# Performance work log

Measured on AMD Instinct MI355X. Metric: run time of the kernel, lower is better.

## Reference

```python
import jax, jax.numpy as jnp
import numpy as np

MIN_SPARSITY = 0.05
MAX_SPARSITY = 0.3


def setup_inputs() -> dict:
    key = jax.random.key(0)
    k1, k2, k3 = jax.random.split(key, 3)
    B, D = 4096, 4096
    H = D // 4
    x = jax.random.normal(k1, (B, D), dtype=jnp.float32)
    W1 = jax.random.normal(k2, (D, H), dtype=jnp.float32) * (1.0 / np.sqrt(D))
    b1 = jnp.zeros((H,), dtype=jnp.float32)
    W2 = jax.random.normal(k3, (H, 1), dtype=jnp.float32) * (1.0 / np.sqrt(H))
    b2 = jnp.zeros((1,), dtype=jnp.float32)
    return {"x": x, "W1": W1, "b1": b1, "W2": W2, "b2": b2}


def reference(x, W1, b1, W2, b2):
    B, D = x.shape
    # learned per-row sparsity in [min, max]
    h = jax.nn.relu(x @ W1 + b1)                      # [B, D//4]
    s = jax.nn.sigmoid(h @ W2 + b2)                   # [B, 1]
    sparsity = MIN_SPARSITY + (MAX_SPARSITY - MIN_SPARSITY) * s  # [B, 1]

    # per-row kth smallest |x| as threshold; k = max(1, round(D*(1-sparsity)))
    abs_x = jnp.abs(x)
    sorted_abs = jnp.sort(abs_x, axis=1)              # [B, D] ascending
    k = jnp.round(D * (1.0 - sparsity[:, 0])).astype(jnp.int32)
    k = jnp.clip(k, 1, D)
    threshold = jnp.take_along_axis(sorted_abs, (k - 1)[:, None], axis=1)  # [B, 1]

    mask = (abs_x > threshold).astype(x.dtype)        # [B, D]
    sparse_x = x * mask
    actual_sparsity = mask.sum(axis=1) / D            # [B]
    l1_reg = jnp.abs(sparse_x).sum(axis=1).mean()     # scalar
    return sparse_x, mask, sparsity, actual_sparsity, l1_reg
```

## Files before the change

### kernel.cpp

```cpp
#include <hip/hip_runtime.h>
#include <hip/hip_fp8.h>

typedef __attribute__((ext_vector_type(4))) float f32x4;


__device__ __forceinline__ unsigned char f2fp8(float f) {
    return (unsigned char)__hip_cvt_float_to_fp8(f, __HIP_SATFINITE, __HIP_E4M3);
}

__device__ __forceinline__ void gl16(const void* g, void* l) {
    __builtin_amdgcn_global_load_lds(
        (const __attribute__((address_space(1))) void*)g,
        (__attribute__((address_space(3))) void*)l, 16, 0, 0);
}

__global__ __launch_bounds__(256) void k0a_cvtx(const float* __restrict__ x,
                                                unsigned char* __restrict__ xa_t)
{
    const int bm = blockIdx.x;
    const int ktbase = blockIdx.y * 16;
    const int t = threadIdx.x;
    const int rr = t >> 2, q = t & 3;
    const int kgp = q ^ ((rr >> 1) & 3);
    const size_t rowoff = (size_t)(bm * 64 + rr) * 4096;

    #pragma unroll
    for (int i = 0; i < 16; i++) {
        const int kt = ktbase + i;
        const float* src = x + rowoff + kt * 32 + q * 8;
        float4 v0 = *(const float4*)src;
        float4 v1 = *(const float4*)(src + 4);
        union { unsigned char c[8]; uint2 u; } o;
        o.c[0] = f2fp8(v0.x); o.c[1] = f2fp8(v0.y);
        o.c[2] = f2fp8(v0.z); o.c[3] = f2fp8(v0.w);
        o.c[4] = f2fp8(v1.x); o.c[5] = f2fp8(v1.y);
        o.c[6] = f2fp8(v1.z); o.c[7] = f2fp8(v1.w);
        *(uint2*)(xa_t + ((size_t)(bm * 128 + kt) * 64 + rr) * 32 + kgp * 8) = o.u;
    }
}

__global__ __launch_bounds__(256) void k0b_cvtw(const float* __restrict__ W1,
                                                unsigned char* __restrict__ wb_t)
{
    __shared__ float ls[32][128];
    const int bx = blockIdx.x;
    const int bn = bx >> 7, kt = bx & 127;
    const int t = threadIdx.x;

    #pragma unroll
    for (int i = 0; i < 4; i++) {
        int s = t + i * 256;
        int r = s >> 5, c4 = s & 31;
        *(float4*)&ls[r][c4 * 4] =
            *(const float4*)(W1 + (size_t)(kt * 32 + r) * 1024 + bn * 128 + c4 * 4);
    }
    __syncthreads();

    const int n = t >> 1, half = t & 1;
    #pragma unroll
    for (int kg2 = 0; kg2 < 2; kg2++) {
        const int kg = half * 2 + kg2;
        const int kgp = kg ^ ((n >> 1) & 3);
        union { unsigned char c[8]; uint2 u; } o;
        #pragma unroll
        for (int j = 0; j < 8; j++) o.c[j] = f2fp8(ls[kg * 8 + j][n] * 64.0f);
        *(uint2*)(wb_t + (size_t)(bn * 128 + kt) * 4096 + n * 32 + kgp * 8) = o.u;
    }
}

__global__ __launch_bounds__(256, 2) void k1est(const unsigned char* __restrict__ xa_t,
                                                const unsigned char* __restrict__ wb_t,
                                                const float* __restrict__ b1,
                                                const float* __restrict__ W2,
                                                float* __restrict__ plogit)
{
    __shared__ alignas(16) unsigned char Ab[4][4096];
    __shared__ alignas(16) unsigned char Bb[4][8192];

    const int bid = blockIdx.x;
    const int wgid = (bid & 7) * 64 + (bid >> 3);
    const int bn = wgid >> 6, bm = wgid & 63;
    const int tid = threadIdx.x;
    const int l = tid & 63, w = tid >> 6;
    const int arow = l & 15, kg = l >> 4;
    const int kgs = kg ^ ((arow >> 1) & 3);

    const unsigned char* abase = xa_t + (size_t)bm * 128 * 2048;
    const unsigned char* bbase = wb_t + (size_t)bn * 128 * 4096;

    f32x4 acc[8];
    #pragma unroll
    for (int j = 0; j < 8; j++) acc[j] = (f32x4)0.0f;

#define ISSUE(step, buf)                                                          \
    do {                                                                          \
        gl16(abase + (size_t)(step) * 4096 + tid * 16, &Ab[buf][tid * 16]);       \
        gl16(bbase + (size_t)(step) * 8192 + tid * 16, &Bb[buf][tid * 16]);       \
        gl16(bbase + (size_t)(step) * 8192 + (256 + tid) * 16,                    \
             &Bb[buf][(256 + tid) * 16]);                                         \
    } while (0)

    ISSUE(0, 0);
    ISSUE(1, 1);

    for (int t = 0; t < 64; t++) {
        const int buf = t & 3;
        if (t <= 61) {
            ISSUE(t + 2, (t + 2) & 3);
            asm volatile("s_waitcnt vmcnt(6)" ::: "memory");
        } else if (t == 62) {
            asm volatile("s_waitcnt vmcnt(3)" ::: "memory");
        } else {
            asm volatile("s_waitcnt vmcnt(0)" ::: "memory");
        }
        __builtin_amdgcn_s_barrier();
        __builtin_amdgcn_sched_barrier(0);

        #pragma unroll
        for (int j = 0; j < 2; j++) {
            long af = *(const long*)&Ab[buf][j * 2048 + (w * 16 + arow) * 32 + kgs * 8];
            #pragma unroll
            for (int nf = 0; nf < 8; nf++) {
                long bf = *(const long*)&Bb[buf][j * 4096 + (nf * 16 + arow) * 32 + kgs * 8];
                acc[nf] = __builtin_amdgcn_mfma_f32_16x16x32_fp8_fp8(af, bf, acc[nf], 0, 0, 0);
            }
        }
    }
#undef ISSUE

    float p[4] = {0.0f, 0.0f, 0.0f, 0.0f};
    #pragma unroll
    for (int nf = 0; nf < 8; nf++) {
        const int n = bn * 128 + nf * 16 + arow;
        const float bb = b1[n], ww = W2[n];
        #pragma unroll
        for (int i = 0; i < 4; i++) {
            float h = acc[nf][i] * 0.015625f + bb;
            if (h > 0.0f) p[i] += h * ww;
        }
    }
    #pragma unroll
    for (int i = 0; i < 4; i++) {
        #pragma unroll
        for (int o = 1; o < 16; o <<= 1) p[i] += __shfl_xor(p[i], o, 64);
        if (arow == 0) {
            const int row = bm * 64 + w * 16 + kg * 4 + i;
            plogit[(size_t)row * 8 + bn] = p[i];
        }
    }
}

__global__ __launch_bounds__(256) void k1b_k(const float* __restrict__ plogit,
                                             const float* __restrict__ b2,
                                             int* __restrict__ k_arr,
                                             float* __restrict__ sp_arr)
{
    int row = blockIdx.x * 256 + threadIdx.x;
    float lg = 0.0f;
    #pragma unroll
    for (int t = 0; t < 8; t++) lg += plogit[(size_t)row * 8 + t];
    double s  = 1.0 / (1.0 + exp(-(double)(lg + b2[0])));
    double sp = 0.05 + 0.25 * s;
    int k = (int)rint(4096.0 * (1.0 - sp));
    if (k < 1) k = 1;
    if (k > 4096) k = 4096;
    k_arr[row] = k;
    sp_arr[row] = (float)sp;
}

__global__ __launch_bounds__(256) void k2_row(const float* __restrict__ x,
                                              const int* __restrict__ k_arr,
                                              const float* __restrict__ sp_arr,
                                              float* __restrict__ out_sparse,
                                              float* __restrict__ out_mask,
                                              float* __restrict__ out_spars,
                                              float* __restrict__ out_actual,
                                              double* __restrict__ l1rows)
{
    __shared__ unsigned bits[4096];
    __shared__ unsigned hist[2048];
    __shared__ unsigned wsum[4];
    __shared__ int cnt_w[4];
    __shared__ double l1_w[4];
    __shared__ unsigned sel_s, selexc_s;

    const int row = blockIdx.x;
    const int tid = threadIdx.x;
    const int lane = tid & 63, wid = tid >> 6;
    const float* xr = x + (size_t)row * 4096;

    for (int i = tid; i < 1024; i += 256) {
        uint4 v = ((const uint4*)xr)[i];
        bits[i * 4 + 0] = v.x;
        bits[i * 4 + 1] = v.y;
        bits[i * 4 + 2] = v.z;
        bits[i * 4 + 3] = v.w;
    }
    if (tid == 0) out_spars[row] = sp_arr[row];

    int krem = k_arr[row];
    unsigned prefix = 0;

    for (int i = tid; i < 2048; i += 256) hist[i] = 0;
    __syncthreads();
    for (int i = tid; i < 4096; i += 256)
        atomicAdd(&hist[(bits[i] & 0x7fffffffu) >> 20], 1u);
    __syncthreads();
    {
        const unsigned base = tid * 8;
        unsigned bl[8];
        unsigned v = 0;
        #pragma unroll
        for (int j = 0; j < 8; j++) { bl[j] = hist[base + j]; v += bl[j]; }
        unsigned sc = v;
        #pragma unroll
        for (int o = 1; o < 64; o <<= 1) {
            unsigned n = __shfl_up(sc, o, 64);
            if (lane >= o) sc += n;
        }
        if (lane == 63) wsum[wid] = sc;
        __syncthreads();
        unsigned off = 0;
        for (int ww = 0; ww < wid; ww++) off += wsum[ww];
        sc += off;
        unsigned exc = sc - v;
        if ((int)sc >= krem && (int)exc < krem) {
            unsigned run = exc;
            #pragma unroll
            for (int j = 0; j < 8; j++) {
                if ((int)run < krem && (int)(run + bl[j]) >= krem) {
                    sel_s = base + j; selexc_s = run;
                }
                run += bl[j];
            }
        }
        __syncthreads();
        prefix = sel_s;
        krem -= (int)selexc_s;
        __syncthreads();
    }

    #pragma unroll
    for (int p = 0; p < 3; p++) {
        const int shift = (p == 0) ? 12 : (p == 1) ? 4 : 0;
        const int width = (p == 2) ? 4 : 8;
        const int nb = 1 << width;
        const int topshift = shift + width;
        if (tid < nb) hist[tid] = 0;
        __syncthreads();
        for (int i = tid; i < 4096; i += 256) {
            unsigned a = bits[i] & 0x7fffffffu;
            if ((a >> topshift) == prefix)
                atomicAdd(&hist[(a >> shift) & (nb - 1)], 1u);
        }
        __syncthreads();
        unsigned v = (tid < nb) ? hist[tid] : 0;
        unsigned sc = v;
        #pragma unroll
        for (int o = 1; o < 64; o <<= 1) {
            unsigned n = __shfl_up(sc, o, 64);
            if (lane >= o) sc += n;
        }
        if (lane == 63) wsum[wid] = sc;
        __syncthreads();
        unsigned off = 0;
        for (int ww = 0; ww < wid; ww++) off += wsum[ww];
        sc += off;
        unsigned exc = sc - v;
        if ((int)sc >= krem && (int)exc < krem) { sel_s = (unsigned)tid; selexc_s = exc; }
        __syncthreads();
        prefix = (prefix << width) | sel_s;
        krem -= (int)selexc_s;
        __syncthreads();
    }
    const unsigned thr = prefix;

    int cnt = 0;
    double l1 = 0.0;
    float* os = out_sparse + (size_t)row * 4096;
    float* om = out_mask + (size_t)row * 4096;
    for (int i = tid; i < 1024; i += 256) {
        float4 sv, mv;
        #pragma unroll
        for (int j = 0; j < 4; j++) {
            unsigned b = bits[i * 4 + j];
            unsigned a = b & 0x7fffffffu;
            bool m = a > thr;
            (&sv.x)[j] = m ? __uint_as_float(b) : 0.0f;
            (&mv.x)[j] = m ? 1.0f : 0.0f;
            if (m) { cnt++; l1 += (double)__uint_as_float(a); }
        }
        ((float4*)os)[i] = sv;
        ((float4*)om)[i] = mv;
    }
    #pragma unroll
    for (int o = 32; o > 0; o >>= 1) {
        cnt += __shfl_down(cnt, o, 64);
        l1  += __shfl_down(l1,  o, 64);
    }
    if (lane == 0) { cnt_w[wid] = cnt; l1_w[wid] = l1; }
    __syncthreads();
    if (tid == 0) {
        int c    = cnt_w[0] + cnt_w[1] + cnt_w[2] + cnt_w[3];
        double l = l1_w[0] + l1_w[1] + l1_w[2] + l1_w[3];
        out_actual[row] = (float)c / 4096.0f;
        l1rows[row] = l;
    }
}

__global__ __launch_bounds__(1024) void k3_l1(const double* __restrict__ l1rows,
                                              float* __restrict__ out_l1)
{
    __shared__ double sm[1024];
    int tid = threadIdx.x;
    double s = l1rows[tid] + l1rows[tid + 1024] + l1rows[tid + 2048] + l1rows[tid + 3072];
    sm[tid] = s;
    __syncthreads();
    for (int st = 512; st > 0; st >>= 1) {
        if (tid < st) sm[tid] += sm[tid + st];
        __syncthreads();
    }
    if (tid == 0) out_l1[0] = (float)(sm[0] / 4096.0);
}

extern "C" void kernel_launch(void* const* d_in, const int* in_sizes, int n_in,
                              void* d_out, int out_size, void* d_ws, size_t ws_size,
                              hipStream_t stream)
{
    const float* x  = (const float*)d_in[0];
    const float* W1 = (const float*)d_in[1];
    const float* b1 = (const float*)d_in[2];
    const float* W2 = (const float*)d_in[3];
    const float* b2 = (const float*)d_in[4];

    float* out        = (float*)d_out;
    float* out_sparse = out;
    float* out_mask   = out + 16777216;
    float* out_spars  = out + 33554432;
    float* out_actual = out + 33558528;
    float* out_l1     = out + 33562624;

    unsigned char* xa_t = (unsigned char*)(out);
    unsigned char* wb_t = (unsigned char*)(out + 4194304);

    char* ws = (char*)d_ws;
    float*  plogit = (float*)(ws);
    int*    k_arr  = (int*)(ws + 131072);
    float*  sp_arr = (float*)(ws + 147456);
    double* l1rows = (double*)(ws + 163840);

    k0a_cvtx<<<dim3(64, 8), 256, 0, stream>>>(x, xa_t);
    k0b_cvtw<<<1024, 256, 0, stream>>>(W1, wb_t);
    k1est<<<512, 256, 0, stream>>>(xa_t, wb_t, b1, W2, plogit);
    k1b_k<<<16, 256, 0, stream>>>(plogit, b2, k_arr, sp_arr);
    k2_row<<<4096, 256, 0, stream>>>(x, k_arr, sp_arr, out_sparse, out_mask,
                                     out_spars, out_actual, l1rows);
    k3_l1<<<1, 1024, 0, stream>>>(l1rows, out_l1);
}
```

Before: 126.2 us.

## Fuse k computation into row kernel and compact radix-select candidates

Removes the separate k1b_k launch by having thread 0 of each row block compute the sigmoid, sparsity and k from the partial logits. After the first 11-bit histogram pass, elements falling in the selected bucket are compacted into a 512-entry shared candidate list, so the later refinement passes scan only those candidates instead of all 4096 elements. It falls back to a full scan if there are too many candidates. The row load and the output loop are also vectorised into uint4 LDS accesses. This adds 2KB of LDS per block and an extra compaction pass with a shared atomic counter.

```diff
diff --git a/kernel.cpp b/kernel.cpp
--- a/kernel.cpp
+++ b/kernel.cpp
@@ -150,27 +150,9 @@
     }
 }
 
-__global__ __launch_bounds__(256) void k1b_k(const float* __restrict__ plogit,
-                                             const float* __restrict__ b2,
-                                             int* __restrict__ k_arr,
-                                             float* __restrict__ sp_arr)
-{
-    int row = blockIdx.x * 256 + threadIdx.x;
-    float lg = 0.0f;
-    #pragma unroll
-    for (int t = 0; t < 8; t++) lg += plogit[(size_t)row * 8 + t];
-    double s  = 1.0 / (1.0 + exp(-(double)(lg + b2[0])));
-    double sp = 0.05 + 0.25 * s;
-    int k = (int)rint(4096.0 * (1.0 - sp));
-    if (k < 1) k = 1;
-    if (k > 4096) k = 4096;
-    k_arr[row] = k;
-    sp_arr[row] = (float)sp;
-}
-
 __global__ __launch_bounds__(256) void k2_row(const float* __restrict__ x,
-                                              const int* __restrict__ k_arr,
-                                              const float* __restrict__ sp_arr,
+                                              const float* __restrict__ plogit,
+                                              const float* __restrict__ b2,
                                               float* __restrict__ out_sparse,
                                               float* __restrict__ out_mask,
                                               float* __restrict__ out_spars,
@@ -179,30 +161,41 @@
 {
     __shared__ unsigned bits[4096];
     __shared__ unsigned hist[2048];
+    __shared__ unsigned cand[512];
+    __shared__ unsigned ccnt;
     __shared__ unsigned wsum[4];
     __shared__ int cnt_w[4];
     __shared__ double l1_w[4];
     __shared__ unsigned sel_s, selexc_s;
+    __shared__ int k_s;
 
     const int row = blockIdx.x;
     const int tid = threadIdx.x;
     const int lane = tid & 63, wid = tid >> 6;
     const float* xr = x + (size_t)row * 4096;
 
-    for (int i = tid; i < 1024; i += 256) {
-        uint4 v = ((const uint4*)xr)[i];
-        bits[i * 4 + 0] = v.x;
-        bits[i * 4 + 1] = v.y;
-        bits[i * 4 + 2] = v.z;
-        bits[i * 4 + 3] = v.w;
-    }
-    if (tid == 0) out_spars[row] = sp_arr[row];
-
-    int krem = k_arr[row];
+    for (int i = tid; i < 1024; i += 256)
+        *(uint4*)&bits[i * 4] = ((const uint4*)xr)[i];
+
+    if (tid == 0) {
+        float lg = 0.0f;
+        #pragma unroll
+        for (int t = 0; t < 8; t++) lg += plogit[(size_t)row * 8 + t];
+        double s  = 1.0 / (1.0 + exp(-(double)(lg + b2[0])));
+        double sp = 0.05 + 0.25 * s;
+        int k = (int)rint(4096.0 * (1.0 - sp));
+        if (k < 1) k = 1;
+        if (k > 4096) k = 4096;
+        k_s = k;
+        ccnt = 0;
+        out_spars[row] = (float)sp;
+    }
+    for (int i = tid; i < 2048; i += 256) hist[i] = 0;
+    __syncthreads();
+
+    int krem = k_s;
     unsigned prefix = 0;
 
-    for (int i = tid; i < 2048; i += 256) hist[i] = 0;
-    __syncthreads();
     for (int i = tid; i < 4096; i += 256)
         atomicAdd(&hist[(bits[i] & 0x7fffffffu) >> 20], 1u);
     __syncthreads();
@@ -240,6 +233,17 @@
         __syncthreads();
     }
 
+    for (int i = tid; i < 4096; i += 256) {
+        unsigned a = bits[i] & 0x7fffffffu;
+        if ((a >> 20) == prefix) {
+            unsigned s = atomicAdd(&ccnt, 1u);
+            if (s < 512) cand[s] = a;
+        }
+    }
+    __syncthreads();
+    const int nc = (int)ccnt;
+    const bool usec = (nc <= 512);
+
     #pragma unroll
     for (int p = 0; p < 3; p++) {
         const int shift = (p == 0) ? 12 : (p == 1) ? 4 : 0;
@@ -248,10 +252,18 @@
         const int topshift = shift + width;
         if (tid < nb) hist[tid] = 0;
         __syncthreads();
-        for (int i = tid; i < 4096; i += 256) {
-            unsigned a = bits[i] & 0x7fffffffu;
-            if ((a >> topshift) == prefix)
-                atomicAdd(&hist[(a >> shift) & (nb - 1)], 1u);
+        if (usec) {
+            for (int i = tid; i < nc; i += 256) {
+                unsigned a = cand[i];
+                if ((a >> topshift) == prefix)
+                    atomicAdd(&hist[(a >> shift) & (nb - 1)], 1u);
+            }
+        } else {
+            for (int i = tid; i < 4096; i += 256) {
+                unsigned a = bits[i] & 0x7fffffffu;
+                if ((a >> topshift) == prefix)
+                    atomicAdd(&hist[(a >> shift) & (nb - 1)], 1u);
+            }
         }
         __syncthreads();
         unsigned v = (tid < nb) ? hist[tid] : 0;
@@ -280,10 +292,11 @@
     float* os = out_sparse + (size_t)row * 4096;
     float* om = out_mask + (size_t)row * 4096;
     for (int i = tid; i < 1024; i += 256) {
+        uint4 bv = *(const uint4*)&bits[i * 4];
         float4 sv, mv;
         #pragma unroll
         for (int j = 0; j < 4; j++) {
-            unsigned b = bits[i * 4 + j];
+            unsigned b = (&bv.x)[j];
             unsigned a = b & 0x7fffffffu;
             bool m = a > thr;
             (&sv.x)[j] = m ? __uint_as_float(b) : 0.0f;
@@ -345,15 +358,12 @@
 
     char* ws = (char*)d_ws;
     float*  plogit = (float*)(ws);
-    int*    k_arr  = (int*)(ws + 131072);
-    float*  sp_arr = (float*)(ws + 147456);
-    double* l1rows = (double*)(ws + 163840);
+    double* l1rows = (double*)(ws + 131072);
 
     k0a_cvtx<<<dim3(64, 8), 256, 0, stream>>>(x, xa_t);
     k0b_cvtw<<<1024, 256, 0, stream>>>(W1, wb_t);
     k1est<<<512, 256, 0, stream>>>(xa_t, wb_t, b1, W2, plogit);
-    k1b_k<<<16, 256, 0, stream>>>(plogit, b2, k_arr, sp_arr);
-    k2_row<<<4096, 256, 0, stream>>>(x, k_arr, sp_arr, out_sparse, out_mask,
+    k2_row<<<4096, 256, 0, stream>>>(x, plogit, b2, out_sparse, out_mask,
                                      out_spars, out_actual, l1rows);
     k3_l1<<<1, 1024, 0, stream>>>(l1rows, out_l1);
 }
```

After: 122.3 us. 3.1% less time.
